# Optimization experiments

Measured on AMD Instinct MI355X. Metric: run time of the kernel, lower is better.

Reference implementation:

```python
import jax, jax.numpy as jnp
import numpy as np

NEG_INF = -1e10


def setup_inputs() -> dict:
    key = jax.random.key(0)
    ks = jax.random.split(key, 9)
    B, S, H, E = 64, 4096, 512, 512
    hidden = jax.random.normal(ks[0], (B, H), dtype=jnp.float32)
    encoder_outputs = jax.random.normal(ks[1], (B, S, E), dtype=jnp.float32)
    mask = jax.random.randint(ks[2], (B, S), 0, 2, dtype=jnp.int32)
    s = 1.0 / np.sqrt(H)
    Wq = jax.random.uniform(ks[3], (H, H), jnp.float32, -s, s)
    bq = jax.random.uniform(ks[4], (H,), jnp.float32, -s, s)
    se = 1.0 / np.sqrt(E)
    Wk = jax.random.uniform(ks[5], (E, H), jnp.float32, -se, se)
    bk = jax.random.uniform(ks[6], (H,), jnp.float32, -se, se)
    Wv = jax.random.uniform(ks[7], (H, 1), jnp.float32, -s, s)
    bv = jax.random.uniform(ks[8], (1,), jnp.float32, -s, s)
    return {"hidden": hidden, "encoder_outputs": encoder_outputs, "mask": mask,
            "Wq": Wq, "bq": bq, "Wk": Wk, "bk": bk, "Wv": Wv, "bv": bv}


def reference(hidden, encoder_outputs, mask, Wq, bq, Wk, bk, Wv, bv):
    # query projection: (B, H) -> broadcast over src_len
    q = hidden @ Wq + bq                       # (B, H)
    k = jnp.einsum('bse,eh->bsh', encoder_outputs, Wk) + bk  # (B, S, H)
    energy = jnp.tanh(q[:, None, :] + k)       # (B, S, H)
    scores = jnp.einsum('bsh,h->bs', energy, Wv[:, 0]) + bv[0]  # (B, S)
    scores = jnp.where(mask == 0, NEG_INF, scores)
    attn = jax.nn.softmax(scores, axis=1)      # (B, S)
    context = jnp.einsum('bs,bse->be', attn, encoder_outputs)   # (B, E)
    return context, attn
```

## Files before the change

### kernel.cpp

```cpp
#include <hip/hip_runtime.h>
#include <hip/hip_bf16.h>

#define B_ 64
#define S_ 4096
#define H_ 512
#define E_ 512
#define NEG_INF_ -1e10f

typedef __attribute__((ext_vector_type(8))) short short8;
typedef __attribute__((ext_vector_type(16))) float f32x16;

static __device__ __forceinline__ unsigned short f2bf(float f) {
    union { float f; unsigned u; } v; v.f = f;
    unsigned x = v.u;
    x += 0x7FFFu + ((x >> 16) & 1u);
    return (unsigned short)(x >> 16);
}

static __device__ __forceinline__ unsigned pk2(float lo, float hi) {
    float2 f; f.x = lo; f.y = hi;
    union { __hip_bfloat162 h; unsigned u; } c;
    c.h = __float22bfloat162_rn(f);
    return c.u;
}

static __device__ __forceinline__ void gload_lds16(const void* g, void* l) {
    __builtin_amdgcn_global_load_lds(
        (const __attribute__((address_space(1))) void*)g,
        (__attribute__((address_space(3))) void*)l, 16, 0, 0);
}

__global__ void prep_wkt(const float* __restrict__ wk, unsigned short* __restrict__ wkt) {
    int idx = blockIdx.x * 256 + threadIdx.x;
    int h = idx >> 9, e = idx & 511;
    wkt[idx] = f2bf(wk[e * H_ + h]);
}

__global__ void prep_qb(const float* __restrict__ hidden, const float* __restrict__ wq,
                        const float* __restrict__ bq, const float* __restrict__ bk,
                        float* __restrict__ qb) {
    __shared__ float hid[H_];
    int b = blockIdx.x, t = threadIdx.x;
    hid[t]       = hidden[b * H_ + t];
    hid[t + 256] = hidden[b * H_ + t + 256];
    __syncthreads();
    for (int hh = t; hh < H_; hh += 256) {
        float s = 0.f;
        for (int e = 0; e < H_; ++e) s += hid[e] * wq[e * H_ + hh];
        qb[b * H_ + hh] = s + bq[hh] + bk[hh];
    }
}

__global__ __launch_bounds__(256, 4) void scores_kernel(
    const float* __restrict__ enc, const unsigned short* __restrict__ wkt,
    const float* __restrict__ qb, const float* __restrict__ wv,
    float* __restrict__ part)
{
    __shared__ char lds[49152];

    int id = blockIdx.x;
    int xcd = id & 7, qq = id >> 3;
    int logical = xcd * 1024 + qq;
    int b  = logical >> 7;
    int r  = logical & 127;
    int st = r >> 2, nt = r & 3;
    int s0 = st * 128;

    const int tid  = threadIdx.x;
    const int lane = tid & 63;
    const int wave = tid >> 6;
    const int wr   = wave >> 1;
    const int wc   = wave & 1;
    const int l31  = lane & 31;
    const int g    = lane >> 5;

    const float* encb = enc + ((size_t)b * S_ + s0) * E_;

    auto stageA = [&](int kc, char* buf) {
#pragma unroll
        for (int p = 0; p < 4; ++p) {
            int gi0 = p * 256 + wave * 64;
            char* db = buf + gi0 * 16;
            int gi  = gi0 + lane;
            int wrh = gi >> 9, gi9 = gi & 511;
            int sr  = gi9 >> 4, ss = gi9 & 15;
            int sl  = ss ^ (sr & 15);
            int row = wrh * 64 + (sl >> 3) * 32 + sr;
            const float* gp = encb + (size_t)row * 512 + kc * 32 + (sl & 7) * 4;
            gload_lds16(gp, db);
        }
    };
    auto stageB = [&](int kc, char* buf) {
#pragma unroll
        for (int p = 0; p < 2; ++p) {
            int gi0 = p * 256 + wave * 64;
            char* db = buf + gi0 * 16;
            int gi = gi0 + lane;
            int sn = gi >> 4, ss = gi & 15;
            int sl = ss ^ (sn & 15);
            int n  = (sl >> 2) * 32 + sn;
            const unsigned short* gp = wkt + (size_t)(nt * 128 + n) * 512 + kc * 32 + (sl & 3) * 8;
            gload_lds16(gp, db);
        }
    };

    f32x16 acc[2][2];
#pragma unroll
    for (int mr = 0; mr < 2; ++mr)
#pragma unroll
        for (int nf = 0; nf < 2; ++nf)
#pragma unroll
            for (int e = 0; e < 16; ++e) acc[mr][nf][e] = 0.f;

    stageA(0, lds);
    stageB(0, lds + 32768);

    for (int kc = 0; kc < 16; ++kc) {
        __syncthreads();
        if (kc < 15) {
            stageA(kc + 1, lds + ((kc + 1) & 1) * 16384);
            stageB(kc + 1, lds + 32768 + ((kc + 1) & 1) * 8192);
        }
        const char* Ab = lds + (kc & 1) * 16384 + wr * 8192;
        const char* Bb = lds + 32768 + (kc & 1) * 8192;
#pragma unroll
        for (int ks = 0; ks < 2; ++ks) {
            short8 af[2];
#pragma unroll
            for (int mr = 0; mr < 2; ++mr) {
                int sl0 = mr * 8 + ks * 4 + g * 2;
                float4 r0 = *(const float4*)(Ab + l31 * 256 + ((sl0 ^ (l31 & 15)) << 4));
                float4 r1 = *(const float4*)(Ab + l31 * 256 + (((sl0 + 1) ^ (l31 & 15)) << 4));
                union { short8 s; unsigned u[4]; } u;
                u.u[0] = pk2(r0.x, r0.y); u.u[1] = pk2(r0.z, r0.w);
                u.u[2] = pk2(r1.x, r1.y); u.u[3] = pk2(r1.z, r1.w);
                af[mr] = u.s;
            }
#pragma unroll
            for (int nf = 0; nf < 2; ++nf) {
                int sl = (wc * 2 + nf) * 4 + ks * 2 + g;
                short8 bfr = *(const short8*)(Bb + l31 * 256 + ((sl ^ (l31 & 15)) << 4));
                acc[0][nf] = __builtin_amdgcn_mfma_f32_32x32x16_bf16(af[0], bfr, acc[0][nf], 0, 0, 0);
                acc[1][nf] = __builtin_amdgcn_mfma_f32_32x32x16_bf16(af[1], bfr, acc[1][nf], 0, 0, 0);
            }
        }
    }

    float p[2][16];
#pragma unroll
    for (int nf = 0; nf < 2; ++nf) {
        int col = nt * 128 + wc * 64 + nf * 32 + l31;
        float qv  = qb[b * H_ + col];
        float wvv = wv[col];
#pragma unroll
        for (int mr = 0; mr < 2; ++mr)
#pragma unroll
            for (int e = 0; e < 16; ++e) {
                float x  = qv + acc[mr][nf][e];
                float ex = __expf(2.f * x);
                float th = 1.f - 2.f / (ex + 1.f);
                float v  = wvv * th;
                p[mr][e] = nf ? (p[mr][e] + v) : v;
            }
    }

    __syncthreads();
    float* ps = (float*)lds;
#pragma unroll
    for (int mr = 0; mr < 2; ++mr)
#pragma unroll
        for (int e = 0; e < 16; ++e) {
            int row = mr * 32 + (e & 3) + 8 * (e >> 2) + 4 * g;
            ps[(wave * 64 + row) * 36 + l31] = p[mr][e];
        }
    __syncthreads();
    float rsum = 0.f;
    {
        const float* myrow = ps + (size_t)(wave * 64 + lane) * 36;
#pragma unroll
        for (int j = 0; j < 8; ++j) {
            float4 v = *(const float4*)(myrow + j * 4);
            rsum += (v.x + v.y) + (v.z + v.w);
        }
    }
    float* pf = (float*)(lds + 36864);
    pf[wave * 64 + lane] = rsum;
    __syncthreads();
    if (tid < 128) {
        int wr2 = tid >> 6, rr = tid & 63;
        float v = pf[(wr2 * 2 + 0) * 64 + rr] + pf[(wr2 * 2 + 1) * 64 + rr];
        int s = s0 + wr2 * 64 + rr;
        part[((size_t)b * S_ + s) * 4 + nt] = v;
    }
}

__global__ void softmax_kernel(const float* __restrict__ part, const int* __restrict__ mask,
                               const float* __restrict__ bvp, float* __restrict__ attn) {
    __shared__ float red[8];
    int b = blockIdx.x, tid = threadIdx.x;
    int wid = tid >> 6, lane = tid & 63;
    float bv0 = bvp[0];
    float vals[8];
    float mx = -3.4e38f;
#pragma unroll
    for (int i = 0; i < 8; ++i) {
        int s = i * 512 + tid;
        float4 v = *(const float4*)(part + ((size_t)b * S_ + s) * 4);
        float sc = (v.x + v.y) + (v.z + v.w) + bv0;
        sc = mask[(size_t)b * S_ + s] ? sc : NEG_INF_;
        vals[i] = sc;
        mx = fmaxf(mx, sc);
    }
#pragma unroll
    for (int off = 1; off < 64; off <<= 1) mx = fmaxf(mx, __shfl_xor(mx, off));
    if (lane == 0) red[wid] = mx;
    __syncthreads();
    mx = red[0];
#pragma unroll
    for (int w = 1; w < 8; ++w) mx = fmaxf(mx, red[w]);
    __syncthreads();
    float sum = 0.f;
#pragma unroll
    for (int i = 0; i < 8; ++i) { vals[i] = __expf(vals[i] - mx); sum += vals[i]; }
#pragma unroll
    for (int off = 1; off < 64; off <<= 1) sum += __shfl_xor(sum, off);
    if (lane == 0) red[wid] = sum;
    __syncthreads();
    sum = red[0] + red[1] + red[2] + red[3] + red[4] + red[5] + red[6] + red[7];
    float inv = 1.f / sum;
#pragma unroll
    for (int i = 0; i < 8; ++i) attn[(size_t)b * S_ + i * 512 + tid] = vals[i] * inv;
}

__global__ void ctx_partial(const float* __restrict__ attn, const float* __restrict__ enc,
                            float* __restrict__ part) {
    __shared__ float a[256];
    int c = blockIdx.x, b = blockIdx.y, t = threadIdx.x;
    a[t] = attn[(size_t)b * S_ + c * 256 + t];
    __syncthreads();
    const float* ep = enc + (size_t)b * S_ * E_ + (size_t)c * 256 * E_ + t * 2;
    float x = 0.f, y = 0.f;
#pragma unroll 4
    for (int s = 0; s < 256; ++s) {
        float2 v = *(const float2*)(ep + (size_t)s * E_);
        x += a[s] * v.x;
        y += a[s] * v.y;
    }
    float* o = part + ((size_t)c * B_ + b) * E_ + t * 2;
    o[0] = x; o[1] = y;
}

__global__ void ctx_reduce(const float* __restrict__ part, float* __restrict__ ctx) {
    int idx = blockIdx.x * 256 + threadIdx.x;
    float s = 0.f;
#pragma unroll
    for (int c = 0; c < 16; ++c) s += part[(size_t)c * (B_ * E_) + idx];
    ctx[idx] = s;
}

extern "C" void kernel_launch(void* const* d_in, const int* in_sizes, int n_in,
                              void* d_out, int out_size, void* d_ws, size_t ws_size,
                              hipStream_t stream) {
    const float* hidden = (const float*)d_in[0];
    const float* enc    = (const float*)d_in[1];
    const int*   mask   = (const int*)d_in[2];
    const float* Wq     = (const float*)d_in[3];
    const float* bq     = (const float*)d_in[4];
    const float* Wk     = (const float*)d_in[5];
    const float* bk     = (const float*)d_in[6];
    const float* Wv     = (const float*)d_in[7];
    const float* bv     = (const float*)d_in[8];

    float* out  = (float*)d_out;
    char*  ws   = (char*)d_ws;
    float*          qbuf   = (float*)ws;
    unsigned short* wkt    = (unsigned short*)(ws + 131072);
    float*          pscore = (float*)(ws + 655360);
    float*          cpart  = (float*)(ws + 655360);

    float* ctx  = out;
    float* attn = out + B_ * E_;

    prep_wkt<<<1024, 256, 0, stream>>>(Wk, wkt);
    prep_qb<<<64, 256, 0, stream>>>(hidden, Wq, bq, bk, qbuf);
    scores_kernel<<<8192, 256, 0, stream>>>(enc, wkt, qbuf, Wv, pscore);
    softmax_kernel<<<64, 512, 0, stream>>>(pscore, mask, bv, attn);
    ctx_partial<<<dim3(16, 64), 256, 0, stream>>>(attn, enc, cpart);
    ctx_reduce<<<128, 256, 0, stream>>>(cpart, ctx);
}
```

Baseline: 520.9 us.

## Stage encoder tile through registers as bf16 with deeper async pipeline

The fp32 encoder tile is no longer copied straight into LDS and converted on every fragment read. It is now loaded into registers, converted once to bf16, and written to a smaller LDS buffer. Wk tiles move to a triple-buffered async copy with two stages in flight, and the waits use explicit vmcnt/lgkmcnt counts instead of a full sync. The aim is to halve LDS footprint and read traffic for A and to remove repeated conversion work. In exchange it needs more registers for the in-flight loads, so occupancy is lowered to 3 blocks per CU.

Result: faster. 441.9 us (-15.2%).

```diff
diff --git a/kernel.cpp b/kernel.cpp
--- a/kernel.cpp
+++ b/kernel.cpp
@@ -29,6 +29,10 @@
         (const __attribute__((address_space(1))) void*)g,
         (__attribute__((address_space(3))) void*)l, 16, 0, 0);
 }
+
+#define VMCNT6 do { asm volatile("s_waitcnt vmcnt(6)" ::: "memory"); __builtin_amdgcn_sched_barrier(0); } while (0)
+#define VMCNT0 do { asm volatile("s_waitcnt vmcnt(0)" ::: "memory"); __builtin_amdgcn_sched_barrier(0); } while (0)
+#define LGKM0  do { asm volatile("s_waitcnt lgkmcnt(0)" ::: "memory"); __builtin_amdgcn_sched_barrier(0); } while (0)
 
 __global__ void prep_wkt(const float* __restrict__ wk, unsigned short* __restrict__ wkt) {
     int idx = blockIdx.x * 256 + threadIdx.x;
@@ -51,12 +55,12 @@
     }
 }
 
-__global__ __launch_bounds__(256, 4) void scores_kernel(
+__global__ __launch_bounds__(256, 3) void scores_kernel(
     const float* __restrict__ enc, const unsigned short* __restrict__ wkt,
     const float* __restrict__ qb, const float* __restrict__ wv,
     float* __restrict__ part)
 {
-    __shared__ char lds[49152];
+    __shared__ char lds[40960];
 
     int id = blockIdx.x;
     int xcd = id & 7, qq = id >> 3;
@@ -76,18 +80,29 @@
 
     const float* encb = enc + ((size_t)b * S_ + s0) * E_;
 
-    auto stageA = [&](int kc, char* buf) {
-#pragma unroll
-        for (int p = 0; p < 4; ++p) {
-            int gi0 = p * 256 + wave * 64;
-            char* db = buf + gi0 * 16;
-            int gi  = gi0 + lane;
-            int wrh = gi >> 9, gi9 = gi & 511;
-            int sr  = gi9 >> 4, ss = gi9 & 15;
-            int sl  = ss ^ (sr & 15);
-            int row = wrh * 64 + (sl >> 3) * 32 + sr;
-            const float* gp = encb + (size_t)row * 512 + kc * 32 + (sl & 7) * 4;
-            gload_lds16(gp, db);
+    auto loadA = [&](int kc, float4 (&rg)[4]) {
+#pragma unroll
+        for (int j = 0; j < 2; ++j) {
+            int sid = tid * 2 + j;
+            int row = sid >> 2, ksl = sid & 3;
+            const float* p = encb + (size_t)row * 512 + kc * 32 + ksl * 8;
+            rg[j * 2 + 0] = *(const float4*)p;
+            rg[j * 2 + 1] = *(const float4*)(p + 4);
+        }
+    };
+    auto writeA = [&](char* buf, const float4 (&rg)[4]) {
+#pragma unroll
+        for (int j = 0; j < 2; ++j) {
+            int sid = tid * 2 + j;
+            int row = sid >> 2, ksl = sid & 3;
+            int srow = row & 31;
+            int sst  = ((row >> 5) * 4 + ksl) ^ (srow & 15);
+            union { short8 s; unsigned u[4]; } u;
+            u.u[0] = pk2(rg[j * 2].x, rg[j * 2].y);
+            u.u[1] = pk2(rg[j * 2].z, rg[j * 2].w);
+            u.u[2] = pk2(rg[j * 2 + 1].x, rg[j * 2 + 1].y);
+            u.u[3] = pk2(rg[j * 2 + 1].z, rg[j * 2 + 1].w);
+            *(short8*)(buf + srow * 256 + sst * 16) = u.s;
         }
     };
     auto stageB = [&](int kc, char* buf) {
@@ -112,38 +127,46 @@
 #pragma unroll
             for (int e = 0; e < 16; ++e) acc[mr][nf][e] = 0.f;
 
-    stageA(0, lds);
-    stageB(0, lds + 32768);
-
-    for (int kc = 0; kc < 16; ++kc) {
-        __syncthreads();
-        if (kc < 15) {
-            stageA(kc + 1, lds + ((kc + 1) & 1) * 16384);
-            stageB(kc + 1, lds + 32768 + ((kc + 1) & 1) * 8192);
-        }
-        const char* Ab = lds + (kc & 1) * 16384 + wr * 8192;
-        const char* Bb = lds + 32768 + (kc & 1) * 8192;
+    float4 ra[4], rb[4];
+
+    loadA(0, ra); stageB(0, lds + 16384);
+    loadA(1, rb); stageB(1, lds + 16384 + 8192);
+
+    auto iter = [&](int kc, float4 (&rg)[4]) {
+        if (kc < 15) { VMCNT6; } else { VMCNT0; }
+        char* Ab = lds + (kc & 1) * 8192;
+        writeA(Ab, rg);
+        LGKM0;
+        __builtin_amdgcn_s_barrier();
+        __builtin_amdgcn_sched_barrier(0);
+        if (kc < 14) {
+            loadA(kc + 2, rg);
+            stageB(kc + 2, lds + 16384 + ((kc + 2) % 3) * 8192);
+        }
+        const char* Bb = lds + 16384 + (kc % 3) * 8192;
 #pragma unroll
         for (int ks = 0; ks < 2; ++ks) {
-            short8 af[2];
+            short8 af[2], bf[2];
 #pragma unroll
             for (int mr = 0; mr < 2; ++mr) {
-                int sl0 = mr * 8 + ks * 4 + g * 2;
-                float4 r0 = *(const float4*)(Ab + l31 * 256 + ((sl0 ^ (l31 & 15)) << 4));
-                float4 r1 = *(const float4*)(Ab + l31 * 256 + (((sl0 + 1) ^ (l31 & 15)) << 4));
-                union { short8 s; unsigned u[4]; } u;
-                u.u[0] = pk2(r0.x, r0.y); u.u[1] = pk2(r0.z, r0.w);
-                u.u[2] = pk2(r1.x, r1.y); u.u[3] = pk2(r1.z, r1.w);
-                af[mr] = u.s;
+                int slog = (wr * 2 + mr) * 4 + ks * 2 + g;
+                af[mr] = *(const short8*)(Ab + l31 * 256 + ((slog ^ (l31 & 15)) << 4));
             }
 #pragma unroll
             for (int nf = 0; nf < 2; ++nf) {
                 int sl = (wc * 2 + nf) * 4 + ks * 2 + g;
-                short8 bfr = *(const short8*)(Bb + l31 * 256 + ((sl ^ (l31 & 15)) << 4));
-                acc[0][nf] = __builtin_amdgcn_mfma_f32_32x32x16_bf16(af[0], bfr, acc[0][nf], 0, 0, 0);
-                acc[1][nf] = __builtin_amdgcn_mfma_f32_32x32x16_bf16(af[1], bfr, acc[1][nf], 0, 0, 0);
+                bf[nf] = *(const short8*)(Bb + l31 * 256 + ((sl ^ (l31 & 15)) << 4));
             }
-        }
+            acc[0][0] = __builtin_amdgcn_mfma_f32_32x32x16_bf16(af[0], bf[0], acc[0][0], 0, 0, 0);
+            acc[0][1] = __builtin_amdgcn_mfma_f32_32x32x16_bf16(af[0], bf[1], acc[0][1], 0, 0, 0);
+            acc[1][0] = __builtin_amdgcn_mfma_f32_32x32x16_bf16(af[1], bf[0], acc[1][0], 0, 0, 0);
+            acc[1][1] = __builtin_amdgcn_mfma_f32_32x32x16_bf16(af[1], bf[1], acc[1][1], 0, 0, 0);
+        }
+    };
+
+    for (int t2 = 0; t2 < 8; ++t2) {
+        iter(t2 * 2,     ra);
+        iter(t2 * 2 + 1, rb);
     }
 
     float p[2][16];
```
